# Optimization experiments

Measured on AMD Instinct MI355X. Metric: run time of the kernel, lower is better.

The kernel has to match this reference:

```python
import jax, jax.numpy as jnp
import numpy as np

B, NPG, T, DIN, H, NH = 8, 64, 50, 3, 128, 4  # batch, nodes-per-graph, timesteps, input_dim, hidden, heads
NN = B * NPG  # 512 total nodes (= max_nodes in the torch module)
HD = H // NH


def setup_inputs() -> dict:
    key = jax.random.key(0)
    ks = jax.random.split(key, 20)
    s = 0.05
    x = jax.random.normal(ks[0], (T, NN, DIN), jnp.float32)
    adj = (jax.random.uniform(ks[1], (T, NN, NN)) < 0.05).astype(jnp.float32)  # sparse 0/1 adjacency
    ego_mask = jax.random.uniform(ks[2], (B, T, NPG)) < 0.7
    W1 = jax.random.normal(ks[3], (DIN, H), jnp.float32) * s
    b1 = jnp.zeros((H,), jnp.float32)
    W2 = jax.random.normal(ks[4], (H, H), jnp.float32) * s
    b2 = jnp.zeros((H,), jnp.float32)
    Wq = jax.random.normal(ks[5], (NN, H, H), jnp.float32) * s
    bq = jax.random.normal(ks[6], (NN, H), jnp.float32) * s
    Wk = jax.random.normal(ks[7], (NN, H, H), jnp.float32) * s
    bk = jax.random.normal(ks[8], (NN, H), jnp.float32) * s
    Wv = jax.random.normal(ks[9], (NN, H, H), jnp.float32) * s
    bv = jax.random.normal(ks[10], (NN, H), jnp.float32) * s
    W_in = jax.random.normal(ks[11], (NN, 3 * H, H), jnp.float32) * s  # MHA in_proj per node
    b_in = jax.random.normal(ks[12], (NN, 3 * H), jnp.float32) * s
    W_out = jax.random.normal(ks[13], (NN, H, H), jnp.float32) * s  # MHA out_proj per node
    b_out = jax.random.normal(ks[14], (NN, H), jnp.float32) * s
    return dict(x=x, adj=adj, ego_mask=ego_mask, W1=W1, b1=b1, W2=W2, b2=b2,
                Wq=Wq, bq=bq, Wk=Wk, bk=bk, Wv=Wv, bv=bv,
                W_in=W_in, b_in=b_in, W_out=W_out, b_out=b_out)


def _forward(x, adj, ego_mask, W1, b1, W2, b2, Wq, bq, Wk, bk, Wv, bv, W_in, b_in, W_out, b_out):
    # flatten mask: [B,T,NPG] -> [T, B*NPG], matching ego_mask.permute(1,0,2).reshape(T,-1)
    mf = jnp.transpose(ego_mask, (1, 0, 2)).reshape(T, NN).astype(x.dtype)
    eye = jnp.eye(NN, dtype=x.dtype)
    # masked adjacency + self loops on ego nodes only (GCNConv add_self_loops on the masked subgraph)
    Ahat = adj * mf[:, :, None] * mf[:, None, :] + eye[None] * mf[:, :, None]  # [T,NN,NN]
    deg = Ahat.sum(axis=1)  # column sums (PyG scatters edge weights on dst)
    dinv = jnp.where(deg > 0, 1.0 / jnp.sqrt(jnp.where(deg > 0, deg, 1.0)), 0.0)  # [T,NN]

    def gcn(X, W, b):
        # out = D^{-1/2} Ahat^T D^{-1/2} X W + b (bias only on ego nodes; others stay zero)
        h = (X @ W) * dinv[..., None]
        h = jnp.einsum('tij,tif->tjf', Ahat, h) * dinv[..., None]
        return h + mf[..., None] * b

    h = jax.nn.relu(gcn(x, W1, b1))
    h = gcn(h, W2, b2)                      # [T, NN, H]; zeros at non-ego -> x_placeholder
    emb = jnp.transpose(h, (1, 0, 2))       # [NN, T, H]

    def lin(e, W, b):  # per-node Linear: e @ W^T + b
        return jnp.einsum('nth,noh->nto', e, W) + b[:, None, :]

    q = lin(emb, Wq, bq)
    k = lin(emb, Wk, bk)
    v = lin(emb, Wv, bv)
    WQ, WK, WV = jnp.split(W_in, 3, axis=1)
    bQ, bK, bV = jnp.split(b_in, 3, axis=1)
    qh = lin(q, WQ, bQ).reshape(NN, T, NH, HD) * (HD ** -0.5)
    kh = lin(k, WK, bK).reshape(NN, T, NH, HD)
    vh = lin(v, WV, bV).reshape(NN, T, NH, HD)
    attn = jax.nn.softmax(jnp.einsum('nqhd,nkhd->nhqk', qh, kh), axis=-1)
    o = jnp.einsum('nhqk,nkhd->nqhd', attn, vh).reshape(NN, T, H)
    out = jnp.einsum('nth,noh->nto', o, W_out) + b_out[:, None, :]  # MHA out_proj
    return out.reshape(B, NPG, T, H)


def reference(x, adj, ego_mask, W1, b1, W2, b2, Wq, bq, Wk, bk, Wv, bv, W_in, b_in, W_out, b_out):
    return _forward(x, adj, ego_mask, W1, b1, W2, b2, Wq, bq, Wk, bk, Wv, bv, W_in, b_in, W_out, b_out)
```

## Files before the change

kernel.cpp:

```cpp
#include <hip/hip_runtime.h>
#include <hip/hip_bf16.h>
#include <cstddef>

#define TT 50
#define NN 512
#define DIN 3
#define HH 128
#define NPG 64
#define DEGCAP 128

typedef short short8 __attribute__((ext_vector_type(8)));
typedef float f32x4 __attribute__((ext_vector_type(4)));

#define SROW 136
#define VROW 56
#define PROW 72
#define SQ_OFF 0
#define SK_OFF 6800
#define SV_OFF 13600
#define PQ_OFF 20784
#define SMEM_NA 39216
#define XW_WOFF 17408
#define SMEM_X 34816

static __device__ __forceinline__ unsigned short f2b(float f) {
    unsigned int u = __builtin_bit_cast(unsigned int, f);
    unsigned int r = (u + 0x7fffu + ((u >> 16) & 1u)) >> 16;
    return (unsigned short)r;
}
static __device__ __forceinline__ float b2f(unsigned short h) {
    unsigned int u = ((unsigned int)h) << 16;
    return __builtin_bit_cast(float, u);
}

static __device__ __forceinline__ void block_sync() {
    __builtin_amdgcn_sched_barrier(0);
    asm volatile("s_waitcnt lgkmcnt(0)");
    __builtin_amdgcn_s_barrier();
    __builtin_amdgcn_sched_barrier(0);
}

static __device__ __forceinline__ short8 cvt2(float4 a, float4 b) {
    short8 t;
    t[0] = (short)f2b(a.x); t[1] = (short)f2b(a.y);
    t[2] = (short)f2b(a.z); t[3] = (short)f2b(a.w);
    t[4] = (short)f2b(b.x); t[5] = (short)f2b(b.y);
    t[6] = (short)f2b(b.z); t[7] = (short)f2b(b.w);
    return t;
}

__global__ __launch_bounds__(256) void mf_kernel(
    const int* __restrict__ ego, float* __restrict__ MF)
{
    const int idx = blockIdx.x * 256 + threadIdx.x;
    const int t = idx >> 9;
    const int i = idx & 511;
    const int b = i >> 6, p = i & 63;
    MF[idx] = (ego[b * (TT * NPG) + t * NPG + p] != 0) ? 1.0f : 0.0f;
}

__global__ __launch_bounds__(256) void edge_kernel(
    const float* __restrict__ adj, const float* __restrict__ MF,
    int* __restrict__ CNT, unsigned short* __restrict__ IDX)
{
    const int bid = blockIdx.x;
    const int t = bid >> 4;
    const int r0 = (bid & 15) * 32;
    const int tid = threadIdx.x;

    __shared__ float mfS[NN];
    for (int j = tid; j < NN; j += 256) mfS[j] = MF[t * NN + j];
    __syncthreads();

    const int half = tid >> 7;
    const int l = tid & 127;

    for (int rr = 0; rr < 32; rr += 2) {
        const int i = r0 + rr + half;
        if (mfS[i] == 0.0f) continue;
        const float4 a4 = *reinterpret_cast<const float4*>(
            &adj[(size_t)t * NN * NN + (size_t)i * NN + l * 4]);
        const float av[4] = {a4.x, a4.y, a4.z, a4.w};
        const int jbase = l * 4;
#pragma unroll
        for (int u = 0; u < 4; ++u) {
            const int j = jbase + u;
            if (av[u] != 0.0f && mfS[j] != 0.0f) {
                int pos = atomicAdd(&CNT[t * NN + j], 1);
                if (pos < DEGCAP)
                    IDX[((size_t)t * NN + j) * DEGCAP + pos] = (unsigned short)i;
            }
        }
    }
}

__global__ __launch_bounds__(256) void dinv_kernel(
    const float* __restrict__ MF, const int* __restrict__ CNT,
    float* __restrict__ DINV)
{
    const int idx = blockIdx.x * 256 + threadIdx.x;
    DINV[idx] = (MF[idx] != 0.0f) ? rsqrtf((float)CNT[idx] + 1.0f) : 0.0f;
}

__global__ __launch_bounds__(256) void xw1_kernel(
    const float* __restrict__ x, const float* __restrict__ W1,
    const float* __restrict__ DINV, unsigned short* __restrict__ XW16)
{
    const int idx = blockIdx.x * 256 + threadIdx.x;
    const int t = idx >> 16;
    const int r = idx & 65535;
    const int i = r >> 7;
    const int f = r & 127;
    const float* xp = x + ((size_t)t * NN + i) * DIN;
    float v = xp[0] * W1[f] + xp[1] * W1[HH + f] + xp[2] * W1[2 * HH + f];
    XW16[idx] = f2b(v * DINV[t * NN + i]);
}

__global__ __launch_bounds__(128) void agg_kernel(
    const unsigned short* __restrict__ XW16, const float* __restrict__ MF,
    const float* __restrict__ DINV, const int* __restrict__ CNT,
    const unsigned short* __restrict__ IDX, const float* __restrict__ bias,
    unsigned short* __restrict__ OUT16, int do_relu)
{
    const int bid = blockIdx.x;
    const int t = bid / NN;
    const int j = bid - t * NN;
    const int f = threadIdx.x;

    __shared__ unsigned short sidx[DEGCAP];

    const float mfj = MF[t * NN + j];
    int cnt = 0;
    if (mfj != 0.0f) cnt = min(CNT[t * NN + j], DEGCAP);
    const unsigned short* lst = IDX + ((size_t)t * NN + j) * DEGCAP;
    for (int k = f; k < cnt; k += 128) sidx[k] = lst[k];
    __syncthreads();

    float outv = 0.0f;
    if (mfj != 0.0f) {
        const unsigned short* base = XW16 + (size_t)t * NN * HH;
        float a0 = b2f(base[j * HH + f]), a1 = 0.0f, a2 = 0.0f, a3 = 0.0f;
        float a4 = 0.0f, a5 = 0.0f, a6 = 0.0f, a7 = 0.0f;
        int k = 0;
        for (; k + 8 <= cnt; k += 8) {
            a0 += b2f(base[(int)sidx[k]     * HH + f]);
            a1 += b2f(base[(int)sidx[k + 1] * HH + f]);
            a2 += b2f(base[(int)sidx[k + 2] * HH + f]);
            a3 += b2f(base[(int)sidx[k + 3] * HH + f]);
            a4 += b2f(base[(int)sidx[k + 4] * HH + f]);
            a5 += b2f(base[(int)sidx[k + 5] * HH + f]);
            a6 += b2f(base[(int)sidx[k + 6] * HH + f]);
            a7 += b2f(base[(int)sidx[k + 7] * HH + f]);
        }
        for (; k + 2 <= cnt; k += 2) {
            a0 += b2f(base[(int)sidx[k]     * HH + f]);
            a1 += b2f(base[(int)sidx[k + 1] * HH + f]);
        }
        if (k < cnt) a2 += b2f(base[(int)sidx[k] * HH + f]);
        outv = DINV[t * NN + j] * (((a0 + a1) + (a2 + a3)) + ((a4 + a5) + (a6 + a7))) + bias[f];
        if (do_relu) outv = fmaxf(outv, 0.0f);
    }
    OUT16[(size_t)t * NN * HH + j * HH + f] = f2b(outv);
}

__global__ __launch_bounds__(256) void xw2_kernel(
    const unsigned short* __restrict__ H16, const float* __restrict__ W2,
    const float* __restrict__ DINV, unsigned short* __restrict__ XW16)
{
    __shared__ unsigned short sm[SMEM_X];
    const int r0 = blockIdx.x * 128;
    const int tid = threadIdx.x;
    const int lane = tid & 63;
    const int wid = tid >> 6;
    const int g = lane >> 4, c = lane & 15;
    const int nt0 = 2 * wid;

#pragma unroll
    for (int it = 0; it < 8; ++it) {
        const int idx = it * 256 + tid;
        const int row = idx >> 4, h8 = (idx & 15) * 8;
        *reinterpret_cast<short8*>(&sm[row * SROW + h8]) =
            *reinterpret_cast<const short8*>(&H16[(size_t)(r0 + row) * HH + h8]);
    }
#pragma unroll
    for (int it = 0; it < 16; ++it) {
        const int flat = it * 1024 + tid * 4;
        float4 w = *reinterpret_cast<const float4*>(W2 + flat);
        const int h = flat >> 7, f0 = flat & 127;
        sm[XW_WOFF + (f0 + 0) * SROW + h] = f2b(w.x);
        sm[XW_WOFF + (f0 + 1) * SROW + h] = f2b(w.y);
        sm[XW_WOFF + (f0 + 2) * SROW + h] = f2b(w.z);
        sm[XW_WOFF + (f0 + 3) * SROW + h] = f2b(w.w);
    }
    __syncthreads();

    f32x4 acc[8][2];
#pragma unroll
    for (int m = 0; m < 8; ++m)
#pragma unroll
        for (int i = 0; i < 2; ++i) acc[m][i] = (f32x4)(0.0f);

#pragma unroll
    for (int kb = 0; kb < 4; ++kb) {
        short8 bf[2];
#pragma unroll
        for (int i = 0; i < 2; ++i)
            bf[i] = *reinterpret_cast<const short8*>(
                &sm[XW_WOFF + (16 * (nt0 + i) + c) * SROW + kb * 32 + 8 * g]);
#pragma unroll
        for (int m = 0; m < 8; ++m) {
            short8 af = *reinterpret_cast<const short8*>(
                &sm[(16 * m + c) * SROW + kb * 32 + 8 * g]);
#pragma unroll
            for (int i = 0; i < 2; ++i)
                acc[m][i] = __builtin_amdgcn_mfma_f32_16x16x32_bf16(af, bf[i], acc[m][i], 0, 0, 0);
        }
    }

#pragma unroll
    for (int m = 0; m < 8; ++m)
#pragma unroll
        for (int r = 0; r < 4; ++r) {
            const int row = 16 * m + 4 * g + r;
            const float dv = DINV[r0 + row];
#pragma unroll
            for (int i = 0; i < 2; ++i)
                XW16[(size_t)(r0 + row) * HH + 16 * (nt0 + i) + c] = f2b(acc[m][i][r] * dv);
        }
}

template<int MODE>
__device__ __forceinline__ void stage(
    unsigned short* __restrict__ sm, int in_off, int out_off,
    const float* __restrict__ W, const float* __restrict__ bias,
    float* __restrict__ gout)
{
    const int tid = threadIdx.x;
    const int lane = tid & 63;
    const int wid = tid >> 6;
    const int g = lane >> 4, c = lane & 15;
    const int nt0 = 2 * wid;

    const float bv0 = bias[16 * nt0 + c];
    const float bv1 = bias[16 * nt0 + 16 + c];

    short8 bf[2][4];
#pragma unroll
    for (int i = 0; i < 2; ++i) {
        const float* wr = W + (16 * (nt0 + i) + c) * HH + 8 * g;
#pragma unroll
        for (int kb = 0; kb < 4; ++kb) {
            float4 w0 = *reinterpret_cast<const float4*>(wr + kb * 32);
            float4 w1 = *reinterpret_cast<const float4*>(wr + kb * 32 + 4);
            bf[i][kb] = cvt2(w0, w1);
        }
    }

    f32x4 acc[4][2];
#pragma unroll
    for (int m = 0; m < 4; ++m)
#pragma unroll
        for (int i = 0; i < 2; ++i) acc[m][i] = (f32x4)(0.0f);

#pragma unroll
    for (int kb = 0; kb < 4; ++kb) {
        short8 af[4];
#pragma unroll
        for (int m = 0; m < 4; ++m)
            af[m] = *reinterpret_cast<const short8*>(
                &sm[in_off + (16 * m + c) * SROW + kb * 32 + 8 * g]);
#pragma unroll
        for (int m = 0; m < 4; ++m)
#pragma unroll
            for (int i = 0; i < 2; ++i)
                acc[m][i] = __builtin_amdgcn_mfma_f32_16x16x32_bf16(af[m], bf[i][kb], acc[m][i], 0, 0, 0);
    }
    block_sync();

    constexpr float scale = 0.17677669529663687f;
#pragma unroll
    for (int m = 0; m < 4; ++m)
#pragma unroll
        for (int i = 0; i < 2; ++i)
#pragma unroll
            for (int r = 0; r < 4; ++r) {
                const int row = 16 * m + 4 * g + r;
                if (row >= TT) continue;
                float v = acc[m][i][r] + (i ? bv1 : bv0);
                if (MODE == 1) v *= scale;
                const int col = 16 * (nt0 + i) + c;
                if (MODE == 3)      gout[row * HH + col] = v;
                else if (MODE == 2) sm[out_off + col * VROW + row] = f2b(v);
                else                sm[out_off + row * SROW + col] = f2b(v);
            }
    block_sync();
}

__global__ __launch_bounds__(256) void node_attn_kernel(
    const unsigned short* __restrict__ EMB16,
    const float* __restrict__ Wq, const float* __restrict__ bq,
    const float* __restrict__ Wk, const float* __restrict__ bk,
    const float* __restrict__ Wv, const float* __restrict__ bv,
    const float* __restrict__ W_in, const float* __restrict__ b_in,
    const float* __restrict__ W_out, const float* __restrict__ b_out,
    float* __restrict__ out)
{
    __shared__ unsigned short sm[SMEM_NA];
    const int n = blockIdx.x;
    const int tid = threadIdx.x;
    const int lane = tid & 63;
    const int wid = tid >> 6;
    const int g = lane >> 4, c = lane & 15;

    for (int idx = tid; idx < HH * 6 + 16; idx += 256) {
        if (idx < HH * 6) {
            int d = idx / 6, cc = idx - d * 6;
            sm[SV_OFF + d * VROW + TT + cc] = 0;
        } else {
            sm[SV_OFF + HH * VROW + (idx - HH * 6)] = 0;
        }
    }

    for (int idx = tid; idx < TT * (HH / 8); idx += 256) {
        int t = idx >> 4, h8 = (idx & 15) * 8;
        *reinterpret_cast<short8*>(&sm[PQ_OFF + t * SROW + h8]) =
            *reinterpret_cast<const short8*>(&EMB16[((size_t)t * NN + n) * HH + h8]);
    }
    block_sync();

    const size_t nHH = (size_t)n * HH * HH;
    const size_t n3HH = (size_t)n * 3 * HH * HH;

    stage<0>(sm, PQ_OFF, SQ_OFF, Wq + nHH, bq + (size_t)n * HH, nullptr);
    stage<0>(sm, PQ_OFF, SK_OFF, Wk + nHH, bk + (size_t)n * HH, nullptr);
    stage<0>(sm, PQ_OFF, SV_OFF, Wv + nHH, bv + (size_t)n * HH, nullptr);
    stage<1>(sm, SQ_OFF, SQ_OFF, W_in + n3HH,                b_in + (size_t)n * 3 * HH,          nullptr);
    stage<0>(sm, SK_OFF, SK_OFF, W_in + n3HH + HH * HH,      b_in + (size_t)n * 3 * HH + HH,     nullptr);
    stage<2>(sm, SV_OFF, SV_OFF, W_in + n3HH + 2 * HH * HH,  b_in + (size_t)n * 3 * HH + 2 * HH, nullptr);

    const int hd = wid;

    f32x4 sacc[4][4];
#pragma unroll
    for (int m = 0; m < 4; ++m)
#pragma unroll
        for (int j = 0; j < 4; ++j) sacc[m][j] = (f32x4)(0.0f);

    short8 aq[4], bk8[4];
#pragma unroll
    for (int m = 0; m < 4; ++m)
        aq[m] = *reinterpret_cast<const short8*>(&sm[SQ_OFF + (16 * m + c) * SROW + hd * 32 + 8 * g]);
#pragma unroll
    for (int j = 0; j < 4; ++j)
        bk8[j] = *reinterpret_cast<const short8*>(&sm[SK_OFF + (16 * j + c) * SROW + hd * 32 + 8 * g]);
#pragma unroll
    for (int m = 0; m < 4; ++m)
#pragma unroll
        for (int j = 0; j < 4; ++j)
            sacc[m][j] = __builtin_amdgcn_mfma_f32_16x16x32_bf16(aq[m], bk8[j], sacc[m][j], 0, 0, 0);

    const bool mask3 = (c >= 2);
    unsigned short* Pbase = &sm[PQ_OFF + hd * 64 * PROW];
#pragma unroll
    for (int m = 0; m < 4; ++m)
#pragma unroll
        for (int r = 0; r < 4; ++r) {
            float v0 = sacc[m][0][r], v1 = sacc[m][1][r], v2 = sacc[m][2][r];
            float v3 = mask3 ? -3.0e38f : sacc[m][3][r];
            float mx = fmaxf(fmaxf(v0, v1), fmaxf(v2, v3));
            mx = fmaxf(mx, __shfl_xor(mx, 1, 16));
            mx = fmaxf(mx, __shfl_xor(mx, 2, 16));
            mx = fmaxf(mx, __shfl_xor(mx, 4, 16));
            mx = fmaxf(mx, __shfl_xor(mx, 8, 16));
            float e0 = __expf(v0 - mx), e1 = __expf(v1 - mx), e2 = __expf(v2 - mx);
            float e3 = mask3 ? 0.0f : __expf(v3 - mx);
            float sum_ = e0 + e1 + e2 + e3;
            sum_ += __shfl_xor(sum_, 1, 16);
            sum_ += __shfl_xor(sum_, 2, 16);
            sum_ += __shfl_xor(sum_, 4, 16);
            sum_ += __shfl_xor(sum_, 8, 16);
            float inv = 1.0f / sum_;
            const int q = 16 * m + 4 * g + r;
            unsigned short* pr = Pbase + q * PROW;
            pr[c]      = f2b(e0 * inv);
            pr[16 + c] = f2b(e1 * inv);
            pr[32 + c] = f2b(e2 * inv);
            pr[48 + c] = f2b(e3 * inv);
        }
    block_sync();

    f32x4 pacc[2][4];
#pragma unroll
    for (int mtd = 0; mtd < 2; ++mtd)
#pragma unroll
        for (int ntq = 0; ntq < 4; ++ntq) pacc[mtd][ntq] = (f32x4)(0.0f);

#pragma unroll
    for (int kb = 0; kb < 2; ++kb) {
        short8 av[2], bp[4];
#pragma unroll
        for (int mtd = 0; mtd < 2; ++mtd)
            av[mtd] = *reinterpret_cast<const short8*>(&sm[SV_OFF + (hd * 32 + 16 * mtd + c) * VROW + kb * 32 + 8 * g]);
#pragma unroll
        for (int ntq = 0; ntq < 4; ++ntq)
            bp[ntq] = *reinterpret_cast<const short8*>(&sm[PQ_OFF + hd * 64 * PROW + (16 * ntq + c) * PROW + kb * 32 + 8 * g]);
#pragma unroll
        for (int mtd = 0; mtd < 2; ++mtd)
#pragma unroll
            for (int ntq = 0; ntq < 4; ++ntq)
                pacc[mtd][ntq] = __builtin_amdgcn_mfma_f32_16x16x32_bf16(av[mtd], bp[ntq], pacc[mtd][ntq], 0, 0, 0);
    }

#pragma unroll
    for (int mtd = 0; mtd < 2; ++mtd)
#pragma unroll
        for (int ntq = 0; ntq < 4; ++ntq)
#pragma unroll
            for (int r = 0; r < 4; ++r) {
                const int q = 16 * ntq + c;
                if (q < TT)
                    sm[SQ_OFF + q * SROW + hd * 32 + 16 * mtd + 4 * g + r] = f2b(pacc[mtd][ntq][r]);
            }
    block_sync();

    stage<3>(sm, SQ_OFF, 0, W_out + nHH, b_out + (size_t)n * HH, out + (size_t)n * TT * HH);
}

extern "C" void kernel_launch(void* const* d_in, const int* in_sizes, int n_in,
                              void* d_out, int out_size, void* d_ws, size_t ws_size,
                              hipStream_t stream)
{
    const float* x     = (const float*)d_in[0];
    const float* adj   = (const float*)d_in[1];
    const int*   ego   = (const int*)d_in[2];
    const float* W1    = (const float*)d_in[3];
    const float* b1    = (const float*)d_in[4];
    const float* W2    = (const float*)d_in[5];
    const float* b2    = (const float*)d_in[6];
    const float* Wq    = (const float*)d_in[7];
    const float* bq    = (const float*)d_in[8];
    const float* Wk    = (const float*)d_in[9];
    const float* bk    = (const float*)d_in[10];
    const float* Wv    = (const float*)d_in[11];
    const float* bv    = (const float*)d_in[12];
    const float* W_in  = (const float*)d_in[13];
    const float* b_in  = (const float*)d_in[14];
    const float* W_out = (const float*)d_in[15];
    const float* b_out = (const float*)d_in[16];
    float* out = (float*)d_out;

    char* ws = (char*)d_ws;
    float*          MF    = (float*)(ws + 0);
    float*          DINV  = (float*)(ws + 102400);
    int*            CNT   = (int*)(ws + 204800);
    unsigned short* IDX   = (unsigned short*)(ws + 307200);
    unsigned short* XW16  = (unsigned short*)(ws + 6860800);
    unsigned short* H16   = (unsigned short*)(ws + 13414400);
    unsigned short* EMB16 = (unsigned short*)(ws + 19968000);

    hipMemsetAsync(CNT, 0, TT * NN * sizeof(int), stream);
    mf_kernel<<<dim3(100), dim3(256), 0, stream>>>(ego, MF);
    edge_kernel<<<dim3(TT * 16), dim3(256), 0, stream>>>(adj, MF, CNT, IDX);
    dinv_kernel<<<dim3(100), dim3(256), 0, stream>>>(MF, CNT, DINV);
    xw1_kernel<<<dim3(12800), dim3(256), 0, stream>>>(x, W1, DINV, XW16);
    agg_kernel<<<dim3(TT * NN), dim3(128), 0, stream>>>(XW16, MF, DINV, CNT, IDX, b1, H16, 1);
    xw2_kernel<<<dim3(200), dim3(256), 0, stream>>>(H16, W2, DINV, XW16);
    agg_kernel<<<dim3(TT * NN), dim3(128), 0, stream>>>(XW16, MF, DINV, CNT, IDX, b2, EMB16, 0);
    node_attn_kernel<<<dim3(NN), dim3(256), 0, stream>>>(EMB16, Wq, bq, Wk, bk, Wv, bv,
                                                         W_in, b_in, W_out, b_out, out);
}
```

Measured before the change: 160.2 us.

## Fuse first-layer feature transform into aggregation and fold CNT reset into mask kernel

Removes the standalone xw1 kernel, which wrote a bf16 XW buffer of T*NN*128 elements. The first GCN layer now recomputes x·W1·dinv per neighbour inside the aggregation kernel, using W1 staged in shared memory. The separate memset of CNT is replaced by zeroing inside mf_kernel, and edge_kernel is split into twice as many blocks of 16 rows each for more parallelism. The trade is redundant 3-term dot products and scattered loads of x and DINV per neighbour, in exchange for one fewer launch and much less global traffic.

```diff
diff --git a/kernel.cpp b/kernel.cpp
--- a/kernel.cpp
+++ b/kernel.cpp
@@ -50,13 +50,14 @@
 }
 
 __global__ __launch_bounds__(256) void mf_kernel(
-    const int* __restrict__ ego, float* __restrict__ MF)
+    const int* __restrict__ ego, float* __restrict__ MF, int* __restrict__ CNT)
 {
     const int idx = blockIdx.x * 256 + threadIdx.x;
     const int t = idx >> 9;
     const int i = idx & 511;
     const int b = i >> 6, p = i & 63;
     MF[idx] = (ego[b * (TT * NPG) + t * NPG + p] != 0) ? 1.0f : 0.0f;
+    CNT[idx] = 0;
 }
 
 __global__ __launch_bounds__(256) void edge_kernel(
@@ -64,8 +65,8 @@
     int* __restrict__ CNT, unsigned short* __restrict__ IDX)
 {
     const int bid = blockIdx.x;
-    const int t = bid >> 4;
-    const int r0 = (bid & 15) * 32;
+    const int t = bid >> 5;
+    const int r0 = (bid & 31) * 16;
     const int tid = threadIdx.x;
 
     __shared__ float mfS[NN];
@@ -75,7 +76,7 @@
     const int half = tid >> 7;
     const int l = tid & 127;
 
-    for (int rr = 0; rr < 32; rr += 2) {
+    for (int rr = 0; rr < 16; rr += 2) {
         const int i = r0 + rr + half;
         if (mfS[i] == 0.0f) continue;
         const float4 a4 = *reinterpret_cast<const float4*>(
@@ -102,18 +103,55 @@
     DINV[idx] = (MF[idx] != 0.0f) ? rsqrtf((float)CNT[idx] + 1.0f) : 0.0f;
 }
 
-__global__ __launch_bounds__(256) void xw1_kernel(
+__global__ __launch_bounds__(128) void agg1_kernel(
     const float* __restrict__ x, const float* __restrict__ W1,
-    const float* __restrict__ DINV, unsigned short* __restrict__ XW16)
-{
-    const int idx = blockIdx.x * 256 + threadIdx.x;
-    const int t = idx >> 16;
-    const int r = idx & 65535;
-    const int i = r >> 7;
-    const int f = r & 127;
-    const float* xp = x + ((size_t)t * NN + i) * DIN;
-    float v = xp[0] * W1[f] + xp[1] * W1[HH + f] + xp[2] * W1[2 * HH + f];
-    XW16[idx] = f2b(v * DINV[t * NN + i]);
+    const float* __restrict__ MF, const float* __restrict__ DINV,
+    const int* __restrict__ CNT, const unsigned short* __restrict__ IDX,
+    const float* __restrict__ b1, unsigned short* __restrict__ H16)
+{
+    const int bid = blockIdx.x;
+    const int t = bid / NN;
+    const int j = bid - t * NN;
+    const int f = threadIdx.x;
+
+    __shared__ float W1S[3 * HH];
+    __shared__ unsigned short sidx[DEGCAP];
+
+    W1S[f] = W1[f];
+    W1S[HH + f] = W1[HH + f];
+    W1S[2 * HH + f] = W1[2 * HH + f];
+
+    const float mfj = MF[t * NN + j];
+    int cnt = 0;
+    if (mfj != 0.0f) cnt = min(CNT[t * NN + j], DEGCAP);
+    const unsigned short* lst = IDX + ((size_t)t * NN + j) * DEGCAP;
+    if (f < cnt) sidx[f] = lst[f];
+    __syncthreads();
+
+    float outv = 0.0f;
+    if (mfj != 0.0f) {
+        const float* xt = x + (size_t)t * NN * DIN;
+        const float* dv = DINV + t * NN;
+        const float w0 = W1S[f], w1 = W1S[HH + f], w2 = W1S[2 * HH + f];
+
+        float a0 = (xt[j * 3] * w0 + xt[j * 3 + 1] * w1 + xt[j * 3 + 2] * w2) * dv[j];
+        float a1 = 0.0f, a2 = 0.0f, a3 = 0.0f;
+        int k = 0;
+        for (; k + 4 <= cnt; k += 4) {
+            const int i0 = sidx[k], i1 = sidx[k + 1], i2 = sidx[k + 2], i3 = sidx[k + 3];
+            a0 += (xt[i0 * 3] * w0 + xt[i0 * 3 + 1] * w1 + xt[i0 * 3 + 2] * w2) * dv[i0];
+            a1 += (xt[i1 * 3] * w0 + xt[i1 * 3 + 1] * w1 + xt[i1 * 3 + 2] * w2) * dv[i1];
+            a2 += (xt[i2 * 3] * w0 + xt[i2 * 3 + 1] * w1 + xt[i2 * 3 + 2] * w2) * dv[i2];
+            a3 += (xt[i3 * 3] * w0 + xt[i3 * 3 + 1] * w1 + xt[i3 * 3 + 2] * w2) * dv[i3];
+        }
+        for (; k < cnt; ++k) {
+            const int i0 = sidx[k];
+            a0 += (xt[i0 * 3] * w0 + xt[i0 * 3 + 1] * w1 + xt[i0 * 3 + 2] * w2) * dv[i0];
+        }
+        outv = dv[j] * ((a0 + a1) + (a2 + a3)) + b1[f];
+        outv = fmaxf(outv, 0.0f);
+    }
+    H16[(size_t)t * NN * HH + j * HH + f] = f2b(outv);
 }
 
 __global__ __launch_bounds__(128) void agg_kernel(
@@ -133,7 +171,7 @@
     int cnt = 0;
     if (mfj != 0.0f) cnt = min(CNT[t * NN + j], DEGCAP);
     const unsigned short* lst = IDX + ((size_t)t * NN + j) * DEGCAP;
-    for (int k = f; k < cnt; k += 128) sidx[k] = lst[k];
+    if (f < cnt) sidx[f] = lst[f];
     __syncthreads();
 
     float outv = 0.0f;
@@ -458,12 +496,10 @@
     unsigned short* H16   = (unsigned short*)(ws + 13414400);
     unsigned short* EMB16 = (unsigned short*)(ws + 19968000);
 
-    hipMemsetAsync(CNT, 0, TT * NN * sizeof(int), stream);
-    mf_kernel<<<dim3(100), dim3(256), 0, stream>>>(ego, MF);
-    edge_kernel<<<dim3(TT * 16), dim3(256), 0, stream>>>(adj, MF, CNT, IDX);
+    mf_kernel<<<dim3(100), dim3(256), 0, stream>>>(ego, MF, CNT);
+    edge_kernel<<<dim3(TT * 32), dim3(256), 0, stream>>>(adj, MF, CNT, IDX);
     dinv_kernel<<<dim3(100), dim3(256), 0, stream>>>(MF, CNT, DINV);
-    xw1_kernel<<<dim3(12800), dim3(256), 0, stream>>>(x, W1, DINV, XW16);
-    agg_kernel<<<dim3(TT * NN), dim3(128), 0, stream>>>(XW16, MF, DINV, CNT, IDX, b1, H16, 1);
+    agg1_kernel<<<dim3(TT * NN), dim3(128), 0, stream>>>(x, W1, MF, DINV, CNT, IDX, b1, H16);
     xw2_kernel<<<dim3(200), dim3(256), 0, stream>>>(H16, W2, DINV, XW16);
     agg_kernel<<<dim3(TT * NN), dim3(128), 0, stream>>>(XW16, MF, DINV, CNT, IDX, b2, EMB16, 0);
     node_attn_kernel<<<dim3(NN), dim3(256), 0, stream>>>(EMB16, Wq, bq, Wk, bk, Wv, bv,
```

After: 139.0 us. 13.2% less time.
